# Kernel tuning notes

Measured on AMD Instinct MI355X. Metric: run time of the kernel, lower is better.

The kernel has to match this reference:

```python
import jax, jax.numpy as jnp
import numpy as np

C = 512  # channels
B, S = 8, 2048


def setup_inputs() -> dict:
    key = jax.random.key(0)
    ks = jax.random.split(key, 8)
    x = jax.random.normal(ks[0], (B, S, C), dtype=jnp.float32)
    eigenvalues = jax.random.normal(ks[1], (B, S), dtype=jnp.float32)
    init = 1.0 / np.sqrt(C)
    Wq = jax.random.normal(ks[2], (C, C), dtype=jnp.float32) * init
    bq = jnp.zeros((C,), dtype=jnp.float32)
    Wk = jax.random.normal(ks[3], (C, C), dtype=jnp.float32) * init
    bk = jnp.zeros((C,), dtype=jnp.float32)
    Wv = jax.random.normal(ks[4], (C, C), dtype=jnp.float32) * init
    bv = jnp.zeros((C,), dtype=jnp.float32)
    return {"x": x, "eigenvalues": eigenvalues, "Wq": Wq, "bq": bq,
            "Wk": Wk, "bk": bk, "Wv": Wv, "bv": bv}


def reference(x, eigenvalues, Wq, bq, Wk, bk, Wv, bv):
    # torch nn.Linear: y = x @ W^T + b
    scale = 1.0 / np.sqrt(x.shape[-1])
    Q = jnp.einsum('bsc,dc->bsd', x, Wq) + bq
    K = jnp.einsum('bsc,dc->bsd', x, Wk) + bk
    V = jnp.einsum('bsc,dc->bsd', x, Wv) + bv
    # scores: [B, S(query), S(key)]
    scores = jnp.einsum('bqd,bkd->bqk', Q, K) * scale
    eigen_weight = jax.nn.sigmoid(eigenvalues)          # [B, S]
    scores = scores * eigen_weight[:, None, :]          # scale per key position
    attn = jax.nn.softmax(scores, axis=-1)
    return jnp.einsum('bqk,bkd->bqd', attn, V)
```

## Files before the change

kernel.cpp:

```cpp
#include <hip/hip_runtime.h>

typedef unsigned short u16;
using bf16x8 = __attribute__((ext_vector_type(8))) short;
using f32x4  = __attribute__((ext_vector_type(4))) float;

__device__ __forceinline__ u16 f2b(float f) {
    __bf16 h = (__bf16)f;
    return __builtin_bit_cast(unsigned short, h);
}
__device__ __forceinline__ float b2f(u16 u) {
    return (float)__builtin_bit_cast(__bf16, u);
}
__device__ __forceinline__ void gload16(const u16* g, const u16* l) {
    __builtin_amdgcn_global_load_lds(
        (const __attribute__((address_space(1))) unsigned int*)g,
        (__attribute__((address_space(3))) unsigned int*)l, 16, 0, 0);
}
__device__ __forceinline__ int swz(int row, int q) { return q ^ ((row ^ (row >> 2)) & 3); }

template<int MODE, int NBLK>
__global__ __launch_bounds__(512, 2)
void gemm8(const u16* __restrict__ A, const u16* __restrict__ B,
           void* __restrict__ Cv, const float* __restrict__ aux,
           float* __restrict__ rowsum,
           int K, int lda, int ldb, int ldc,
           long strA, long strB, long strC, long strAux, long strRS)
{
    constexpr int BR  = NBLK * 64;
    constexpr int VMC = (NBLK == 4) ? 6 : 5;
    __shared__ __align__(16) u16 sA[2][2][256 * 32];
    __shared__ __align__(16) u16 sB[2][2][BR * 32];

    const int tid  = threadIdx.x;
    const int lane = tid & 63;
    const int wave = tid >> 6;
    const int wm = wave >> 2, wn = wave & 3;
    const int l16 = lane & 15, qld = lane >> 4;

    const int gx = gridDim.x, gy = gridDim.y;
    const int nxy = gx * gy;
    int li = blockIdx.y * gx + blockIdx.x;
    li = (li & 7) * (nxy >> 3) + (li >> 3);
    const int bx = li % gx, by = li / gx;
    const int bn0 = bx * BR, bm0 = by * 256;
    const long z = blockIdx.z;

    const u16* Ab = A + z * strA + (long)bm0 * lda;
    const u16* Bb = B + z * strB + (long)bn0 * ldb;
    const float* auxp = aux + z * strAux;

    const int cA0 = tid, cA1 = 512 + tid;
    const u16* srcA0 = Ab + (long)(cA0 >> 2) * lda + swz(cA0 >> 2, cA0 & 3) * 8;
    const u16* srcA1 = Ab + (long)(cA1 >> 2) * lda + swz(cA1 >> 2, cA1 & 3) * 8;
    const int cB1 = (NBLK == 4) ? cA1 : cA0;
    const u16* srcB0 = Bb + (long)(cA0 >> 2) * ldb + swz(cA0 >> 2, cA0 & 3) * 8;
    const u16* srcB1 = Bb + (long)(cB1 >> 2) * ldb + swz(cB1 >> 2, cB1 & 3) * 8;
    const int wch = (tid & ~63) * 8;

#define STAGE_A(sl, kh, colb) do { \
    gload16(srcA0 + (colb), &sA[sl][kh][wch]); \
    gload16(srcA1 + (colb), &sA[sl][kh][wch + 4096]); } while (0)
#define STAGE_B(sl, kh, colb) do { \
    gload16(srcB0 + (colb), &sB[sl][kh][wch]); \
    if constexpr (NBLK == 4) { gload16(srcB1 + (colb), &sB[sl][kh][wch + 4096]); } } while (0)

    int offA[8], offB[NBLK];
#pragma unroll
    for (int mf = 0; mf < 8; ++mf) {
        const int row = wm * 128 + mf * 16 + l16;
        offA[mf] = row * 32 + swz(row, qld) * 8;
    }
#pragma unroll
    for (int n = 0; n < NBLK; ++n) {
        const int row = wn * (NBLK * 16) + n * 16 + l16;
        offB[n] = row * 32 + swz(row, qld) * 8;
    }

    f32x4 acc[8][NBLK] = {};
    const int NT = K >> 6;

    STAGE_A(0, 0, 0);
    STAGE_B(0, 0, 0);
    STAGE_A(0, 1, 32);
    STAGE_B(0, 1, 32);
    if (NT > 1) STAGE_A(1, 0, 64);
    asm volatile("s_waitcnt vmcnt(2)" ::: "memory");
    __builtin_amdgcn_sched_barrier(0);
    asm volatile("s_barrier" ::: "memory");

    for (int t = 0; t < NT; ++t) {
        const int s = t & 1, s1 = s ^ 1;
        const int kc1 = (t + 1) << 6;
        const bool i1 = (t + 1 < NT), i2 = (t + 2 < NT);
        const bool tail = (t >= NT - 2);

        bf16x8 afr[4], bfr[NBLK];
#pragma unroll
        for (int j = 0; j < 4; ++j) afr[j] = *(const bf16x8*)&sA[s][0][offA[j]];
#pragma unroll
        for (int n = 0; n < NBLK; ++n) bfr[n] = *(const bf16x8*)&sB[s][0][offB[n]];
        if (i1) STAGE_B(s1, 0, kc1);
        asm volatile("s_barrier" ::: "memory");
        __builtin_amdgcn_s_setprio(1);
#pragma unroll
        for (int j = 0; j < 4; ++j)
#pragma unroll
            for (int n = 0; n < NBLK; ++n)
                acc[j][n] = __builtin_amdgcn_mfma_f32_16x16x32_bf16(afr[j], bfr[n], acc[j][n], 0, 0, 0);
        __builtin_amdgcn_s_setprio(0);
        asm volatile("s_waitcnt lgkmcnt(0)" ::: "memory");
        __builtin_amdgcn_sched_barrier(0);
        asm volatile("s_barrier" ::: "memory");

#pragma unroll
        for (int j = 0; j < 4; ++j) afr[j] = *(const bf16x8*)&sA[s][0][offA[4 + j]];
        if (i1) STAGE_A(s1, 1, kc1 + 32);
        asm volatile("s_barrier" ::: "memory");
        __builtin_amdgcn_s_setprio(1);
#pragma unroll
        for (int j = 0; j < 4; ++j)
#pragma unroll
            for (int n = 0; n < NBLK; ++n)
                acc[4 + j][n] = __builtin_amdgcn_mfma_f32_16x16x32_bf16(afr[j], bfr[n], acc[4 + j][n], 0, 0, 0);
        __builtin_amdgcn_s_setprio(0);
        if (tail) asm volatile("s_waitcnt vmcnt(0)" ::: "memory");
        else      asm volatile("s_waitcnt vmcnt(%0)" :: "i"(VMC) : "memory");
        asm volatile("s_waitcnt lgkmcnt(0)" ::: "memory");
        __builtin_amdgcn_sched_barrier(0);
        asm volatile("s_barrier" ::: "memory");

#pragma unroll
        for (int j = 0; j < 4; ++j) afr[j] = *(const bf16x8*)&sA[s][1][offA[j]];
#pragma unroll
        for (int n = 0; n < NBLK; ++n) bfr[n] = *(const bf16x8*)&sB[s][1][offB[n]];
        if (i1) STAGE_B(s1, 1, kc1 + 32);
        asm volatile("s_barrier" ::: "memory");
        __builtin_amdgcn_s_setprio(1);
#pragma unroll
        for (int j = 0; j < 4; ++j)
#pragma unroll
            for (int n = 0; n < NBLK; ++n)
                acc[j][n] = __builtin_amdgcn_mfma_f32_16x16x32_bf16(afr[j], bfr[n], acc[j][n], 0, 0, 0);
        __builtin_amdgcn_s_setprio(0);
        asm volatile("s_waitcnt lgkmcnt(0)" ::: "memory");
        __builtin_amdgcn_sched_barrier(0);
        asm volatile("s_barrier" ::: "memory");

#pragma unroll
        for (int j = 0; j < 4; ++j) afr[j] = *(const bf16x8*)&sA[s][1][offA[4 + j]];
        if (i2) STAGE_A(s, 0, kc1 + 64);
        asm volatile("s_barrier" ::: "memory");
        __builtin_amdgcn_s_setprio(1);
#pragma unroll
        for (int j = 0; j < 4; ++j)
#pragma unroll
            for (int n = 0; n < NBLK; ++n)
                acc[4 + j][n] = __builtin_amdgcn_mfma_f32_16x16x32_bf16(afr[j], bfr[n], acc[4 + j][n], 0, 0, 0);
        __builtin_amdgcn_s_setprio(0);
        if (tail) asm volatile("s_waitcnt vmcnt(0)" ::: "memory");
        else      asm volatile("s_waitcnt vmcnt(%0)" :: "i"(VMC) : "memory");
        asm volatile("s_waitcnt lgkmcnt(0)" ::: "memory");
        __builtin_amdgcn_sched_barrier(0);
        asm volatile("s_barrier" ::: "memory");
    }
#undef STAGE_A
#undef STAGE_B

    const int rg = lane >> 4;
    const int orow0 = bm0 + wm * 128;
    const int ocol0 = bn0 + wn * (NBLK * 16);

    if constexpr (MODE == 0) {
        u16* Co = (u16*)Cv + z * strC;
        float bias[NBLK];
#pragma unroll
        for (int n = 0; n < NBLK; ++n) bias[n] = auxp[ocol0 + n * 16 + l16];
#pragma unroll
        for (int mf = 0; mf < 8; ++mf)
#pragma unroll
            for (int n = 0; n < NBLK; ++n) {
                const int col = ocol0 + n * 16 + l16;
#pragma unroll
                for (int r = 0; r < 4; ++r) {
                    const int row = orow0 + mf * 16 + rg * 4 + r;
                    Co[(long)row * ldc + col] = f2b(acc[mf][n][r] + bias[n]);
                }
            }
    } else if constexpr (MODE == 2) {
        u16* Co = (u16*)Cv + z * strC;
        float* rsp = rowsum + z * strRS;
        float wkn[NBLK];
#pragma unroll
        for (int n = 0; n < NBLK; ++n) wkn[n] = auxp[ocol0 + n * 16 + l16];
#pragma unroll
        for (int mf = 0; mf < 8; ++mf)
#pragma unroll
            for (int r = 0; r < 4; ++r) {
                const int row = orow0 + mf * 16 + rg * 4 + r;
                float partial = 0.f;
#pragma unroll
                for (int n = 0; n < NBLK; ++n) {
                    const int col = ocol0 + n * 16 + l16;
                    const float p = exp2f(acc[mf][n][r] * wkn[n]);
                    const u16 pb = f2b(p);
                    Co[(long)row * ldc + col] = pb;
                    partial += b2f(pb);
                }
                partial += __shfl_xor(partial, 1);
                partial += __shfl_xor(partial, 2);
                partial += __shfl_xor(partial, 4);
                partial += __shfl_xor(partial, 8);
                if (l16 == 0) atomicAdd(&rsp[row], partial);
            }
    } else {
        float* Co = (float*)Cv + z * strC;
#pragma unroll
        for (int mf = 0; mf < 8; ++mf)
#pragma unroll
            for (int r = 0; r < 4; ++r) {
                const int row = orow0 + mf * 16 + rg * 4 + r;
                const float inv = 1.0f / auxp[row];
#pragma unroll
                for (int n = 0; n < NBLK; ++n) {
                    const int col = ocol0 + n * 16 + l16;
                    Co[(long)row * ldc + col] = acc[mf][n][r] * inv;
                }
            }
    }
}

__global__ void cvt_bf16(const float* __restrict__ in, u16* __restrict__ out, int n4) {
    const int i = blockIdx.x * 256 + threadIdx.x;
    if (i >= n4) return;
    const float4 f = ((const float4*)in)[i];
    ushort4 o;
    o.x = f2b(f.x); o.y = f2b(f.y); o.z = f2b(f.z); o.w = f2b(f.w);
    ((ushort4*)out)[i] = o;
}

__global__ void wk_kernel(const float* __restrict__ eig, float* __restrict__ wk, int n) {
    const int i = blockIdx.x * 256 + threadIdx.x;
    if (i >= n) return;
    const float s = 1.0f / (1.0f + expf(-eig[i]));
    wk[i] = s * (float)(1.4426950408889634 / 22.627416997969522);
}

__global__ __launch_bounds__(256)
void transpose_v(const u16* __restrict__ Vq, u16* __restrict__ Vt) {
    __shared__ u16 t[64][65];
    const int tid = threadIdx.x;
    const int d0  = blockIdx.x * 64;
    const int bs0 = blockIdx.y * 64;
#pragma unroll
    for (int i = 0; i < 16; ++i) {
        const int idx = i * 256 + tid;
        const int r = idx >> 6, c = idx & 63;
        t[r][c] = Vq[(long)(bs0 + r) * 1536 + d0 + c];
    }
    __syncthreads();
    const long b = bs0 >> 11;
    const int s0 = bs0 & 2047;
#pragma unroll
    for (int i = 0; i < 16; ++i) {
        const int idx = i * 256 + tid;
        const int dch = idx >> 6, ss = idx & 63;
        Vt[(b * 512 + d0 + dch) * 2048 + s0 + ss] = t[ss][dch];
    }
}

extern "C" void kernel_launch(void* const* d_in, const int* in_sizes, int n_in,
                              void* d_out, int out_size, void* d_ws, size_t ws_size,
                              hipStream_t stream) {
    const float* x  = (const float*)d_in[0];
    const float* ev = (const float*)d_in[1];
    const float* Wq = (const float*)d_in[2];
    const float* bq = (const float*)d_in[3];
    const float* Wk = (const float*)d_in[4];
    const float* bk = (const float*)d_in[5];
    const float* Wv = (const float*)d_in[6];
    const float* bv = (const float*)d_in[7];
    float* out = (float*)d_out;

    char* ws = (char*)d_ws;
    u16*   P      = (u16*)(ws);
    u16*   xb     = (u16*)(ws + (64ul << 20));
    u16*   qkvC   = (u16*)(ws + (80ul << 20));
    u16*   Vt     = (u16*)(ws + (128ul << 20));
    u16*   Wb     = (u16*)(ws + (144ul << 20));
    float* biasb  = (float*)(ws + (146ul << 20));
    float* wk     = (float*)(ws + (146ul << 20) + 65536);
    float* rowsum = (float*)(ws + (146ul << 20) + 131072);

    cvt_bf16<<<dim3(8192), dim3(256), 0, stream>>>(x, xb, 2097152);
    cvt_bf16<<<dim3(256),  dim3(256), 0, stream>>>(Wq, Wb,          65536);
    cvt_bf16<<<dim3(256),  dim3(256), 0, stream>>>(Wk, Wb + 262144, 65536);
    cvt_bf16<<<dim3(256),  dim3(256), 0, stream>>>(Wv, Wb + 524288, 65536);
    hipMemcpyAsync(biasb,        bq, 512 * 4, hipMemcpyDeviceToDevice, stream);
    hipMemcpyAsync(biasb + 512,  bk, 512 * 4, hipMemcpyDeviceToDevice, stream);
    hipMemcpyAsync(biasb + 1024, bv, 512 * 4, hipMemcpyDeviceToDevice, stream);
    wk_kernel<<<dim3(64), dim3(256), 0, stream>>>(ev, wk, 16384);
    hipMemsetAsync(rowsum, 0, 65536, stream);

    gemm8<0, 2><<<dim3(12, 64, 1), dim3(512), 0, stream>>>(
        xb, Wb, qkvC, biasb, nullptr,
        512, 512, 512, 1536,
        0L, 0L, 0L, 0L, 0L);

    transpose_v<<<dim3(8, 256), dim3(256), 0, stream>>>(qkvC + 1024, Vt);

    gemm8<2, 4><<<dim3(8, 8, 8), dim3(512), 0, stream>>>(
        qkvC, qkvC + 512, P, wk, rowsum,
        512, 1536, 1536, 2048,
        3145728L, 3145728L, 4194304L, 2048L, 2048L);

    gemm8<3, 2><<<dim3(4, 8, 8), dim3(512), 0, stream>>>(
        P, Vt, out, rowsum, nullptr,
        2048, 2048, 2048, 512,
        4194304L, 1048576L, 1048576L, 2048L, 0L);
}
```

Baseline: 269.5 us.

## Restructure GEMM LDS tiles to 64-wide rows with XOR-8 swizzle and new staging

Replaces the split k-half LDS buffers (two 32-column halves with a 2-bit swizzle) with single 64-column rows using an 8-way XOR swizzle on 16-byte chunks. The global-to-LDS staging schedule also changes: A for the next tile is loaded in two chunks during the first two MFMA phases, and B is prefetched two tiles ahead into the slot being consumed. The aim is fewer, larger contiguous global loads per row, bank-conflict-free fragment reads, and a simpler wait pattern. The risks are that issuing B two tiles ahead into the current slot could race with reads of that slot, and that the changed vmcnt accounting could stall or fail to cover in-flight loads.

```diff
diff --git a/kernel.cpp b/kernel.cpp
--- a/kernel.cpp
+++ b/kernel.cpp
@@ -16,7 +16,6 @@
         (const __attribute__((address_space(1))) unsigned int*)g,
         (__attribute__((address_space(3))) unsigned int*)l, 16, 0, 0);
 }
-__device__ __forceinline__ int swz(int row, int q) { return q ^ ((row ^ (row >> 2)) & 3); }
 
 template<int MODE, int NBLK>
 __global__ __launch_bounds__(512, 2)
@@ -26,10 +25,10 @@
            int K, int lda, int ldb, int ldc,
            long strA, long strB, long strC, long strAux, long strRS)
 {
-    constexpr int BR  = NBLK * 64;
-    constexpr int VMC = (NBLK == 4) ? 6 : 5;
-    __shared__ __align__(16) u16 sA[2][2][256 * 32];
-    __shared__ __align__(16) u16 sB[2][2][BR * 32];
+    constexpr int BR = NBLK * 64;
+    constexpr int BROUND = BR / 64;
+    __shared__ __align__(16) u16 sA[2][256 * 64];
+    __shared__ __align__(16) u16 sB[2][BR * 64];
 
     const int tid  = threadIdx.x;
     const int lane = tid & 63;
@@ -49,122 +48,107 @@
     const u16* Bb = B + z * strB + (long)bn0 * ldb;
     const float* auxp = aux + z * strAux;
 
-    const int cA0 = tid, cA1 = 512 + tid;
-    const u16* srcA0 = Ab + (long)(cA0 >> 2) * lda + swz(cA0 >> 2, cA0 & 3) * 8;
-    const u16* srcA1 = Ab + (long)(cA1 >> 2) * lda + swz(cA1 >> 2, cA1 & 3) * 8;
-    const int cB1 = (NBLK == 4) ? cA1 : cA0;
-    const u16* srcB0 = Bb + (long)(cA0 >> 2) * ldb + swz(cA0 >> 2, cA0 & 3) * 8;
-    const u16* srcB1 = Bb + (long)(cB1 >> 2) * ldb + swz(cB1 >> 2, cB1 & 3) * 8;
+    const u16* srcA[4];
+    const u16* srcB[BROUND];
+#pragma unroll
+    for (int i = 0; i < 4; ++i) {
+        const int ci = i * 512 + tid, row = ci >> 3, c = ci & 7;
+        srcA[i] = Ab + (long)row * lda + (c ^ (row & 7)) * 8;
+    }
+#pragma unroll
+    for (int i = 0; i < BROUND; ++i) {
+        const int ci = i * 512 + tid, row = ci >> 3, c = ci & 7;
+        srcB[i] = Bb + (long)row * ldb + (c ^ (row & 7)) * 8;
+    }
     const int wch = (tid & ~63) * 8;
 
-#define STAGE_A(sl, kh, colb) do { \
-    gload16(srcA0 + (colb), &sA[sl][kh][wch]); \
-    gload16(srcA1 + (colb), &sA[sl][kh][wch + 4096]); } while (0)
-#define STAGE_B(sl, kh, colb) do { \
-    gload16(srcB0 + (colb), &sB[sl][kh][wch]); \
-    if constexpr (NBLK == 4) { gload16(srcB1 + (colb), &sB[sl][kh][wch + 4096]); } } while (0)
-
-    int offA[8], offB[NBLK];
-#pragma unroll
-    for (int mf = 0; mf < 8; ++mf) {
-        const int row = wm * 128 + mf * 16 + l16;
-        offA[mf] = row * 32 + swz(row, qld) * 8;
-    }
-#pragma unroll
-    for (int n = 0; n < NBLK; ++n) {
-        const int row = wn * (NBLK * 16) + n * 16 + l16;
-        offB[n] = row * 32 + swz(row, qld) * 8;
-    }
+#define STAGE_A2(sl, kc, i0) do { \
+    gload16(srcA[i0] + (kc),     &sA[sl][(i0) * 4096 + wch]); \
+    gload16(srcA[i0 + 1] + (kc), &sA[sl][(i0 + 1) * 4096 + wch]); } while (0)
+#define STAGE_B(sl, kc) do { \
+    _Pragma("unroll") \
+    for (int i = 0; i < BROUND; ++i) \
+        gload16(srcB[i] + (kc), &sB[sl][i * 4096 + wch]); } while (0)
 
     f32x4 acc[8][NBLK] = {};
     const int NT = K >> 6;
 
-    STAGE_A(0, 0, 0);
-    STAGE_B(0, 0, 0);
-    STAGE_A(0, 1, 32);
-    STAGE_B(0, 1, 32);
-    if (NT > 1) STAGE_A(1, 0, 64);
-    asm volatile("s_waitcnt vmcnt(2)" ::: "memory");
+    auto rdA = [&](int s, int mf, int kh) -> bf16x8 {
+        const int row = wm * 128 + mf * 16 + l16;
+        int byte_off = row * 128 + (kh * 32 + qld * 8) * 2;
+        byte_off ^= (row & 7) << 4;
+        return *(const bf16x8*)((const char*)&sA[s][0] + byte_off);
+    };
+    auto rdB = [&](int s, int n, int kh) -> bf16x8 {
+        const int row = wn * (NBLK * 16) + n * 16 + l16;
+        int byte_off = row * 128 + (kh * 32 + qld * 8) * 2;
+        byte_off ^= (row & 7) << 4;
+        return *(const bf16x8*)((const char*)&sB[s][0] + byte_off);
+    };
+
+#define MFMA_HALF(base) do { \
+    __builtin_amdgcn_s_setprio(1); \
+    _Pragma("unroll") \
+    for (int j = 0; j < 4; ++j) \
+        _Pragma("unroll") \
+        for (int n = 0; n < NBLK; ++n) \
+            acc[(base) + j][n] = __builtin_amdgcn_mfma_f32_16x16x32_bf16(afr[j], bfr[n], acc[(base) + j][n], 0, 0, 0); \
+    __builtin_amdgcn_s_setprio(0); } while (0)
+
+#define BAR()   asm volatile("s_barrier" ::: "memory")
+#define LGKM0() do { asm volatile("s_waitcnt lgkmcnt(0)" ::: "memory"); \
+                     __builtin_amdgcn_sched_barrier(0); } while (0)
+
+    STAGE_A2(0, 0, 0); STAGE_A2(0, 0, 2);
+    STAGE_B(0, 0);
+    STAGE_B(1, 64);
+    asm volatile("s_waitcnt vmcnt(%0)" :: "i"(BROUND) : "memory");
     __builtin_amdgcn_sched_barrier(0);
-    asm volatile("s_barrier" ::: "memory");
+    BAR();
 
     for (int t = 0; t < NT; ++t) {
         const int s = t & 1, s1 = s ^ 1;
-        const int kc1 = (t + 1) << 6;
-        const bool i1 = (t + 1 < NT), i2 = (t + 2 < NT);
-        const bool tail = (t >= NT - 2);
-
         bf16x8 afr[4], bfr[NBLK];
-#pragma unroll
-        for (int j = 0; j < 4; ++j) afr[j] = *(const bf16x8*)&sA[s][0][offA[j]];
-#pragma unroll
-        for (int n = 0; n < NBLK; ++n) bfr[n] = *(const bf16x8*)&sB[s][0][offB[n]];
-        if (i1) STAGE_B(s1, 0, kc1);
-        asm volatile("s_barrier" ::: "memory");
-        __builtin_amdgcn_s_setprio(1);
-#pragma unroll
-        for (int j = 0; j < 4; ++j)
-#pragma unroll
-            for (int n = 0; n < NBLK; ++n)
-                acc[j][n] = __builtin_amdgcn_mfma_f32_16x16x32_bf16(afr[j], bfr[n], acc[j][n], 0, 0, 0);
-        __builtin_amdgcn_s_setprio(0);
-        asm volatile("s_waitcnt lgkmcnt(0)" ::: "memory");
+
+#pragma unroll
+        for (int j = 0; j < 4; ++j) afr[j] = rdA(s, j, 0);
+#pragma unroll
+        for (int n = 0; n < NBLK; ++n) bfr[n] = rdB(s, n, 0);
+        if (t + 1 < NT) STAGE_A2(s1, (t + 1) * 64, 0);
+        BAR(); LGKM0();
+        MFMA_HALF(0);
+        BAR();
+
+#pragma unroll
+        for (int j = 0; j < 4; ++j) afr[j] = rdA(s, 4 + j, 0);
+        if (t + 1 < NT) STAGE_A2(s1, (t + 1) * 64, 2);
+        BAR(); LGKM0();
+        MFMA_HALF(4);
+        BAR();
+
+#pragma unroll
+        for (int j = 0; j < 4; ++j) afr[j] = rdA(s, j, 1);
+#pragma unroll
+        for (int n = 0; n < NBLK; ++n) bfr[n] = rdB(s, n, 1);
+        BAR(); LGKM0();
+        MFMA_HALF(0);
+        BAR();
+
+#pragma unroll
+        for (int j = 0; j < 4; ++j) afr[j] = rdA(s, 4 + j, 1);
+        if (t + 2 < NT) STAGE_B(s, (t + 2) * 64);
+        BAR(); LGKM0();
+        MFMA_HALF(4);
+        if (t + 2 < NT) asm volatile("s_waitcnt vmcnt(%0)" :: "i"(BROUND) : "memory");
+        else            asm volatile("s_waitcnt vmcnt(0)" ::: "memory");
         __builtin_amdgcn_sched_barrier(0);
-        asm volatile("s_barrier" ::: "memory");
-
-#pragma unroll
-        for (int j = 0; j < 4; ++j) afr[j] = *(const bf16x8*)&sA[s][0][offA[4 + j]];
-        if (i1) STAGE_A(s1, 1, kc1 + 32);
-        asm volatile("s_barrier" ::: "memory");
-        __builtin_amdgcn_s_setprio(1);
-#pragma unroll
-        for (int j = 0; j < 4; ++j)
-#pragma unroll
-            for (int n = 0; n < NBLK; ++n)
-                acc[4 + j][n] = __builtin_amdgcn_mfma_f32_16x16x32_bf16(afr[j], bfr[n], acc[4 + j][n], 0, 0, 0);
-        __builtin_amdgcn_s_setprio(0);
-        if (tail) asm volatile("s_waitcnt vmcnt(0)" ::: "memory");
-        else      asm volatile("s_waitcnt vmcnt(%0)" :: "i"(VMC) : "memory");
-        asm volatile("s_waitcnt lgkmcnt(0)" ::: "memory");
-        __builtin_amdgcn_sched_barrier(0);
-        asm volatile("s_barrier" ::: "memory");
-
-#pragma unroll
-        for (int j = 0; j < 4; ++j) afr[j] = *(const bf16x8*)&sA[s][1][offA[j]];
-#pragma unroll
-        for (int n = 0; n < NBLK; ++n) bfr[n] = *(const bf16x8*)&sB[s][1][offB[n]];
-        if (i1) STAGE_B(s1, 1, kc1 + 32);
-        asm volatile("s_barrier" ::: "memory");
-        __builtin_amdgcn_s_setprio(1);
-#pragma unroll
-        for (int j = 0; j < 4; ++j)
-#pragma unroll
-            for (int n = 0; n < NBLK; ++n)
-                acc[j][n] = __builtin_amdgcn_mfma_f32_16x16x32_bf16(afr[j], bfr[n], acc[j][n], 0, 0, 0);
-        __builtin_amdgcn_s_setprio(0);
-        asm volatile("s_waitcnt lgkmcnt(0)" ::: "memory");
-        __builtin_amdgcn_sched_barrier(0);
-        asm volatile("s_barrier" ::: "memory");
-
-#pragma unroll
-        for (int j = 0; j < 4; ++j) afr[j] = *(const bf16x8*)&sA[s][1][offA[4 + j]];
-        if (i2) STAGE_A(s, 0, kc1 + 64);
-        asm volatile("s_barrier" ::: "memory");
-        __builtin_amdgcn_s_setprio(1);
-#pragma unroll
-        for (int j = 0; j < 4; ++j)
-#pragma unroll
-            for (int n = 0; n < NBLK; ++n)
-                acc[4 + j][n] = __builtin_amdgcn_mfma_f32_16x16x32_bf16(afr[j], bfr[n], acc[4 + j][n], 0, 0, 0);
-        __builtin_amdgcn_s_setprio(0);
-        if (tail) asm volatile("s_waitcnt vmcnt(0)" ::: "memory");
-        else      asm volatile("s_waitcnt vmcnt(%0)" :: "i"(VMC) : "memory");
-        asm volatile("s_waitcnt lgkmcnt(0)" ::: "memory");
-        __builtin_amdgcn_sched_barrier(0);
-        asm volatile("s_barrier" ::: "memory");
-    }
-#undef STAGE_A
+        BAR();
+    }
+#undef STAGE_A2
 #undef STAGE_B
+#undef MFMA_HALF
+#undef BAR
+#undef LGKM0
 
     const int rg = lane >> 4;
     const int orow0 = bm0 + wm * 128;
```

Result: no change. 272.0 us (+0.9%).
